# Kernel optimization log

Hardware: AMD Instinct MI355X
Metric: run time of the kernel (lower is better)

The kernel has to match this reference:

```python
import jax, jax.numpy as jnp
from jax import lax
import numpy as np

IGNORE_INDEX = -100


def setup_inputs() -> dict:
    key = jax.random.key(0)
    k1, k2, k3 = jax.random.split(key, 3)
    N, D, V = 8192, 2048, 32000
    x = jax.random.normal(k1, (N, D), dtype=jnp.float32) * (D ** -0.5)
    proj_weight = jax.random.normal(k2, (V, D), dtype=jnp.float32) * (D ** -0.5)
    target = jax.random.randint(k3, (N,), 0, V, dtype=jnp.int64 if jax.config.jax_enable_x64 else jnp.int32)
    return {"x": x, "proj_weight": proj_weight, "target": target, "num_splits": 4}


def reference(x, proj_weight, target, num_splits):
    # Fused linear-projection + cross-entropy, chunked over the token dim so the
    # full [N, V] logits tensor is never materialized (only [N/num_splits, V]).
    N, D = x.shape
    chunk = N // num_splits  # N chosen divisible by num_splits
    x_c = x.reshape(num_splits, chunk, D)
    t_c = target.reshape(num_splits, chunk)

    def body(carry, inp):
        loss_sum, count = carry
        xi, ti = inp  # [chunk, D], [chunk]
        logits = jnp.einsum('nd,vd->nv', xi, proj_weight)  # [chunk, V]
        lse = jax.nn.logsumexp(logits, axis=-1)            # [chunk]
        valid = ti != IGNORE_INDEX
        safe_t = jnp.where(valid, ti, 0)
        tgt_logit = jnp.take_along_axis(logits, safe_t[:, None], axis=-1)[:, 0]
        loss = jnp.where(valid, lse - tgt_logit, 0.0)
        return (loss_sum + loss.sum(), count + valid.sum()), None

    init = (jnp.float32(0.0), jnp.int32(0))
    (loss_sum, count), _ = lax.scan(body, init, (x_c, t_c))
    return loss_sum / count.astype(jnp.float32)  # mean over non-ignored tokens
```

## Files before the change

### kernel.cpp

```cpp
#include <hip/hip_runtime.h>
#include <hip/hip_bf16.h>


typedef __bf16 bf16_t;
typedef bf16_t bf16x8 __attribute__((ext_vector_type(8)));
typedef float f32x4 __attribute__((ext_vector_type(4)));

constexpr int N_TOK = 8192;
constexpr int DIM   = 2048;
constexpr int VOCAB = 32000;
constexpr int BM = 256, BN = 256, BK = 64;
constexpr int MT  = N_TOK / BM;
constexpr int NVT = VOCAB / BN;
constexpr int NKT = DIM / BK;
constexpr int IGNORE_INDEX = -100;

#define GPTR(p) ((const __attribute__((address_space(1))) void*)(p))
#define LPTR(p) ((__attribute__((address_space(3))) void*)(p))

#define VMCNT(N)                                            \
  asm volatile("s_waitcnt vmcnt(" #N ")" ::: "memory");     \
  __builtin_amdgcn_sched_barrier(0)
#define LGKM0()                                             \
  asm volatile("s_waitcnt lgkmcnt(0)" ::: "memory");        \
  __builtin_amdgcn_sched_barrier(0)

__device__ __forceinline__ bf16_t f2bf(float f) {
  union { float f; unsigned u; } in; in.f = f;
  unsigned u = in.u;
  unsigned r = u + 0x7fffu + ((u >> 16) & 1u);
  union { unsigned short s; bf16_t b; } out;
  out.s = (unsigned short)(r >> 16);
  return out.b;
}

constexpr int XN8 = N_TOK * DIM / 8;
constexpr int WN8 = VOCAB * DIM / 8;
constexpr int CVT_BLOCKS = 2048;

__global__ __launch_bounds__(256) void cvt_both(const float* __restrict__ x,
                                                const float* __restrict__ w,
                                                bf16_t* __restrict__ xb,
                                                bf16_t* __restrict__ wb) {
  for (int i = blockIdx.x * 256 + threadIdx.x; i < XN8 + WN8; i += CVT_BLOCKS * 256) {
    const float* src; bf16_t* dst; int j;
    if (i < XN8) { src = x; dst = xb; j = i; }
    else { src = w; dst = wb; j = i - XN8; }
    const float4* s = (const float4*)src;
    float4 a = s[2 * (size_t)j], b = s[2 * (size_t)j + 1];
    bf16x8 o;
    o[0] = f2bf(a.x); o[1] = f2bf(a.y); o[2] = f2bf(a.z); o[3] = f2bf(a.w);
    o[4] = f2bf(b.x); o[5] = f2bf(b.y); o[6] = f2bf(b.z); o[7] = f2bf(b.w);
    *(bf16x8*)(dst + (size_t)j * 8) = o;
  }
}

__device__ __forceinline__ void stage_half(const bf16_t* base, int kt,
                                           long toff, char* smem, int ldsoff,
                                           int tid) {
  const bf16_t* g = base + kt * BK + toff;
  __builtin_amdgcn_global_load_lds(GPTR(g), LPTR(smem + ldsoff + tid * 16), 16, 0, 0);
  __builtin_amdgcn_global_load_lds(GPTR(g + 64 * DIM), LPTR(smem + ldsoff + 8192 + tid * 16), 16, 0, 0);
}

template <int SLOT>
__device__ __forceinline__ bf16x8 ldA(const char* smem, int row, int ks, int lg) {
  int ch = (ks * 4 + lg) ^ (row & 7);
  return *(const bf16x8*)(smem + SLOT + row * 128 + ch * 16);
}
template <int SLOT>
__device__ __forceinline__ bf16x8 ldB(const char* smem, int row, int ks, int lg) {
  int ch = (ks * 4 + lg) ^ (row & 7);
  return *(const bf16x8*)(smem + SLOT + 32768 + row * 128 + ch * 16);
}

#define PRE_MFMA()                                    \
  __builtin_amdgcn_s_barrier();                       \
  LGKM0();

#define MFMA_HALF(MOFF)                                                         \
  __builtin_amdgcn_s_setprio(1);                                                \
  _Pragma("unroll") for (int m = 0; m < 4; ++m)                                 \
    _Pragma("unroll") for (int n = 0; n < 4; ++n)                               \
      acc[m + MOFF][n] = __builtin_amdgcn_mfma_f32_16x16x32_bf16(               \
          aq[m], bq[n], acc[m + MOFF][n], 0, 0, 0);                             \
  __builtin_amdgcn_s_setprio(0);

template <int CUR, int NXT>
__device__ __forceinline__ void tile_body(
    const bf16_t* Ab, const bf16_t* Bb, int ktB, int ktA2, long toff,
    char* smem, int tid, int wr, int wc, int l15, int lg, f32x4 (&acc)[8][4]) {
  bf16x8 aq[4], bq[4];
  const int arow = wr * 128 + l15;
  const int brow = wc * 64 + l15;

#pragma unroll
  for (int m = 0; m < 4; ++m) aq[m] = ldA<CUR>(smem, arow + m * 16, 0, lg);
#pragma unroll
  for (int n = 0; n < 4; ++n) bq[n] = ldB<CUR>(smem, brow + n * 16, 0, lg);
  stage_half(Bb, ktB, toff, smem, NXT + 32768, tid);
  VMCNT(4);
  PRE_MFMA();
  MFMA_HALF(0);
  __builtin_amdgcn_s_barrier();

#pragma unroll
  for (int m = 0; m < 4; ++m) aq[m] = ldA<CUR>(smem, arow + 64 + m * 16, 0, lg);
  stage_half(Bb + 128 * DIM, ktB, toff, smem, NXT + 49152, tid);
  PRE_MFMA();
  MFMA_HALF(4);
  __builtin_amdgcn_s_barrier();

#pragma unroll
  for (int m = 0; m < 4; ++m) aq[m] = ldA<CUR>(smem, arow + m * 16, 1, lg);
#pragma unroll
  for (int n = 0; n < 4; ++n) bq[n] = ldB<CUR>(smem, brow + n * 16, 1, lg);
  stage_half(Ab + 128 * DIM, ktB, toff, smem, NXT + 16384, tid);
  PRE_MFMA();
  MFMA_HALF(0);
  __builtin_amdgcn_s_barrier();

#pragma unroll
  for (int m = 0; m < 4; ++m) aq[m] = ldA<CUR>(smem, arow + 64 + m * 16, 1, lg);
  stage_half(Ab, ktA2, toff, smem, CUR, tid);
  VMCNT(4);
  PRE_MFMA();
  MFMA_HALF(4);
  __builtin_amdgcn_s_barrier();
}

__global__ __launch_bounds__(512, 2) void fused_gemm_lse(
    const bf16_t* __restrict__ X, const bf16_t* __restrict__ W,
    const int* __restrict__ target,
    float2* __restrict__ partials, float* __restrict__ tgt_logit) {
  __shared__ __align__(16) char smem[131072];

  const int tid  = threadIdx.x;
  const int lane = tid & 63;
  const int wid  = tid >> 6;
  const int wr   = wid >> 2;
  const int wc   = wid & 3;
  const int l15  = lane & 15;
  const int lg   = lane >> 4;

  int bid  = blockIdx.x;
  int wgid = (bid & 7) * (MT * NVT / 8) + (bid >> 3);
  int mt = wgid & (MT - 1);
  int vt = wgid >> 5;
  const int brow = mt * BM;
  const int bcol = vt * BN;

  const bf16_t* Abase = X + (size_t)brow * DIM;
  const bf16_t* Bbase = W + (size_t)bcol * DIM;

  const int srow = tid >> 3;
  const int ssc  = (tid & 7) ^ (srow & 7);
  const long toff = (long)srow * DIM + ssc * 8;

  f32x4 acc[8][4];
#pragma unroll
  for (int m = 0; m < 8; ++m)
#pragma unroll
    for (int n = 0; n < 4; ++n)
      acc[m][n] = (f32x4){0.f, 0.f, 0.f, 0.f};

  stage_half(Abase,             0, toff, smem, 0,     tid);
  stage_half(Abase + 128 * DIM, 0, toff, smem, 16384, tid);
  stage_half(Bbase,             0, toff, smem, 32768, tid);
  stage_half(Bbase + 128 * DIM, 0, toff, smem, 49152, tid);
  stage_half(Abase,             1, toff, smem, 65536, tid);
  VMCNT(0);
  __builtin_amdgcn_s_barrier();

  for (int t = 0; t < NKT; t += 2) {
    tile_body<0, 65536>(Abase, Bbase, (t + 1) & (NKT - 1), (t + 2) & (NKT - 1),
                        toff, smem, tid, wr, wc, l15, lg, acc);
    tile_body<65536, 0>(Abase, Bbase, (t + 2) & (NKT - 1), (t + 3) & (NKT - 1),
                        toff, smem, tid, wr, wc, l15, lg, acc);
  }

  __syncthreads();
  float* smax = (float*)smem;
  float* ssum = (float*)(smem + 4096);
#pragma unroll
  for (int m = 0; m < 8; ++m) {
#pragma unroll
    for (int i = 0; i < 4; ++i) {
      int rloc = wr * 128 + m * 16 + lg * 4 + i;
      int grow = brow + rloc;
      int tgt  = target[grow];
      float v0 = acc[m][0][i], v1 = acc[m][1][i], v2 = acc[m][2][i], v3 = acc[m][3][i];
      int colbase = bcol + wc * 64 + l15;
      if (colbase      == tgt) tgt_logit[grow] = v0;
      if (colbase + 16 == tgt) tgt_logit[grow] = v1;
      if (colbase + 32 == tgt) tgt_logit[grow] = v2;
      if (colbase + 48 == tgt) tgt_logit[grow] = v3;
      float rmax = fmaxf(fmaxf(v0, v1), fmaxf(v2, v3));
#pragma unroll
      for (int s = 1; s < 16; s <<= 1) rmax = fmaxf(rmax, __shfl_xor(rmax, s));
      float rsum = __expf(v0 - rmax) + __expf(v1 - rmax) +
                   __expf(v2 - rmax) + __expf(v3 - rmax);
#pragma unroll
      for (int s = 1; s < 16; s <<= 1) rsum += __shfl_xor(rsum, s);
      if (l15 == 0) { smax[rloc * 4 + wc] = rmax; ssum[rloc * 4 + wc] = rsum; }
    }
  }
  __syncthreads();
  if (tid < BM) {
    float M = smax[tid * 4], S = ssum[tid * 4];
#pragma unroll
    for (int c = 1; c < 4; ++c) {
      float m2 = smax[tid * 4 + c], s2 = ssum[tid * 4 + c];
      float Mn = fmaxf(M, m2);
      S = S * __expf(M - Mn) + s2 * __expf(m2 - Mn);
      M = Mn;
    }
    partials[(size_t)(brow + tid) * NVT + vt] = make_float2(M, S);
  }
}

__global__ __launch_bounds__(256) void finalize_rows(
    const float2* __restrict__ partials, const float* __restrict__ tgt_logit,
    const int* __restrict__ target, float2* __restrict__ blocksum) {
  int tid = threadIdx.x, lane = tid & 63, w = tid >> 6;
  int row = blockIdx.x * 4 + w;
  float M = -1e30f, S = 0.f;
  for (int i = lane; i < NVT; i += 64) {
    float2 p = partials[(size_t)row * NVT + i];
    float Mn = fmaxf(M, p.x);
    S = S * __expf(M - Mn) + p.y * __expf(p.x - Mn);
    M = Mn;
  }
#pragma unroll
  for (int s = 1; s < 64; s <<= 1) {
    float Mo = __shfl_xor(M, s), So = __shfl_xor(S, s);
    float Mn = fmaxf(M, Mo);
    S = S * __expf(M - Mn) + So * __expf(Mo - Mn);
    M = Mn;
  }
  __shared__ float ls[4], cs[4];
  if (lane == 0) {
    int t = target[row];
    bool valid = (t != IGNORE_INDEX);
    float lse = M + __logf(S);
    ls[w] = valid ? (lse - tgt_logit[row]) : 0.f;
    cs[w] = valid ? 1.f : 0.f;
  }
  __syncthreads();
  if (tid == 0)
    blocksum[blockIdx.x] = make_float2(ls[0] + ls[1] + ls[2] + ls[3],
                                       cs[0] + cs[1] + cs[2] + cs[3]);
}

__global__ __launch_bounds__(256) void finalize_out(
    const float2* __restrict__ blocksum, float* __restrict__ out) {
  int tid = threadIdx.x;
  float s = 0.f, c = 0.f;
  for (int i = tid; i < N_TOK / 4; i += 256) {
    float2 b = blocksum[i];
    s += b.x; c += b.y;
  }
#pragma unroll
  for (int k = 1; k < 64; k <<= 1) { s += __shfl_xor(s, k); c += __shfl_xor(c, k); }
  __shared__ float ss[4], cc[4];
  int w = tid >> 6;
  if ((tid & 63) == 0) { ss[w] = s; cc[w] = c; }
  __syncthreads();
  if (tid == 0) out[0] = (ss[0] + ss[1] + ss[2] + ss[3]) / (cc[0] + cc[1] + cc[2] + cc[3]);
}

extern "C" void kernel_launch(void* const* d_in, const int* in_sizes, int n_in,
                              void* d_out, int out_size, void* d_ws, size_t ws_size,
                              hipStream_t stream) {
  const float* x = (const float*)d_in[0];
  const float* w = (const float*)d_in[1];
  const int* target = (const int*)d_in[2];
  float* out = (float*)d_out;

  char* ws = (char*)d_ws;
  size_t off = 0;
  bf16_t* Xbf = (bf16_t*)(ws + off); off += (size_t)N_TOK * DIM * 2;
  bf16_t* Wbf = (bf16_t*)(ws + off); off += (size_t)VOCAB * DIM * 2;
  float2* partials = (float2*)(ws + off); off += (size_t)N_TOK * NVT * 8;
  float*  tgtlog   = (float*)(ws + off);  off += (size_t)N_TOK * 4;
  float2* blocksum = (float2*)(ws + off); off += (size_t)(N_TOK / 4) * 8;
  (void)ws_size; (void)in_sizes; (void)n_in; (void)out_size;

  cvt_both<<<CVT_BLOCKS, 256, 0, stream>>>(x, w, Xbf, Wbf);
  fused_gemm_lse<<<MT * NVT, 512, 0, stream>>>(Xbf, Wbf, target, partials, tgtlog);
  finalize_rows<<<N_TOK / 4, 256, 0, stream>>>(partials, tgtlog, target, blocksum);
  finalize_out<<<1, 256, 0, stream>>>(blocksum, out);
}
```

Before: 1.441 ms.

## Replace interleaved 4-phase pipeline with simple double-buffered full-tile loads

Replaces the fine-grained four-phase schedule, which interleaved partial LDS reads, half-tile global-to-LDS stages and MFMA groups, with a simpler scheme. Each iteration reads the whole K tile from LDS into registers, issues all 64 MFMAs, then stages the entire next-but-one tile into the freed buffer. Barriers and waitcnt stalls drop from four per tile to one, but register pressure rises (24 bf16x8 fragments held at once) and the overlap between global loads and compute becomes coarser.

New measurement: 1.535 ms. 1.07x slower.

```diff
diff --git a/kernel.cpp b/kernel.cpp
--- a/kernel.cpp
+++ b/kernel.cpp
@@ -74,58 +74,38 @@
   return *(const bf16x8*)(smem + SLOT + 32768 + row * 128 + ch * 16);
 }
 
-#define PRE_MFMA()                                    \
-  __builtin_amdgcn_s_barrier();                       \
+template <int CUR>
+__device__ __forceinline__ void tile_body(
+    const bf16_t* Ab, const bf16_t* Bb, int ktN, long toff, char* smem,
+    int tid, int arow, int brow, int lg, f32x4 (&acc)[8][4]) {
+  bf16x8 a0[8], b0[4], a1[8], b1[4];
+#pragma unroll
+  for (int m = 0; m < 8; ++m) a0[m] = ldA<CUR>(smem, arow + m * 16, 0, lg);
+#pragma unroll
+  for (int n = 0; n < 4; ++n) b0[n] = ldB<CUR>(smem, brow + n * 16, 0, lg);
+#pragma unroll
+  for (int m = 0; m < 8; ++m) a1[m] = ldA<CUR>(smem, arow + m * 16, 1, lg);
+#pragma unroll
+  for (int n = 0; n < 4; ++n) b1[n] = ldB<CUR>(smem, brow + n * 16, 1, lg);
+  __builtin_amdgcn_s_setprio(1);
+#pragma unroll
+  for (int m = 0; m < 8; ++m)
+#pragma unroll
+    for (int n = 0; n < 4; ++n)
+      acc[m][n] = __builtin_amdgcn_mfma_f32_16x16x32_bf16(a0[m], b0[n], acc[m][n], 0, 0, 0);
+#pragma unroll
+  for (int m = 0; m < 8; ++m)
+#pragma unroll
+    for (int n = 0; n < 4; ++n)
+      acc[m][n] = __builtin_amdgcn_mfma_f32_16x16x32_bf16(a1[m], b1[n], acc[m][n], 0, 0, 0);
+  __builtin_amdgcn_s_setprio(0);
   LGKM0();
-
-#define MFMA_HALF(MOFF)                                                         \
-  __builtin_amdgcn_s_setprio(1);                                                \
-  _Pragma("unroll") for (int m = 0; m < 4; ++m)                                 \
-    _Pragma("unroll") for (int n = 0; n < 4; ++n)                               \
-      acc[m + MOFF][n] = __builtin_amdgcn_mfma_f32_16x16x32_bf16(               \
-          aq[m], bq[n], acc[m + MOFF][n], 0, 0, 0);                             \
-  __builtin_amdgcn_s_setprio(0);
-
-template <int CUR, int NXT>
-__device__ __forceinline__ void tile_body(
-    const bf16_t* Ab, const bf16_t* Bb, int ktB, int ktA2, long toff,
-    char* smem, int tid, int wr, int wc, int l15, int lg, f32x4 (&acc)[8][4]) {
-  bf16x8 aq[4], bq[4];
-  const int arow = wr * 128 + l15;
-  const int brow = wc * 64 + l15;
-
-#pragma unroll
-  for (int m = 0; m < 4; ++m) aq[m] = ldA<CUR>(smem, arow + m * 16, 0, lg);
-#pragma unroll
-  for (int n = 0; n < 4; ++n) bq[n] = ldB<CUR>(smem, brow + n * 16, 0, lg);
-  stage_half(Bb, ktB, toff, smem, NXT + 32768, tid);
-  VMCNT(4);
-  PRE_MFMA();
-  MFMA_HALF(0);
   __builtin_amdgcn_s_barrier();
-
-#pragma unroll
-  for (int m = 0; m < 4; ++m) aq[m] = ldA<CUR>(smem, arow + 64 + m * 16, 0, lg);
-  stage_half(Bb + 128 * DIM, ktB, toff, smem, NXT + 49152, tid);
-  PRE_MFMA();
-  MFMA_HALF(4);
-  __builtin_amdgcn_s_barrier();
-
-#pragma unroll
-  for (int m = 0; m < 4; ++m) aq[m] = ldA<CUR>(smem, arow + m * 16, 1, lg);
-#pragma unroll
-  for (int n = 0; n < 4; ++n) bq[n] = ldB<CUR>(smem, brow + n * 16, 1, lg);
-  stage_half(Ab + 128 * DIM, ktB, toff, smem, NXT + 16384, tid);
-  PRE_MFMA();
-  MFMA_HALF(0);
-  __builtin_amdgcn_s_barrier();
-
-#pragma unroll
-  for (int m = 0; m < 4; ++m) aq[m] = ldA<CUR>(smem, arow + 64 + m * 16, 1, lg);
-  stage_half(Ab, ktA2, toff, smem, CUR, tid);
-  VMCNT(4);
-  PRE_MFMA();
-  MFMA_HALF(4);
+  stage_half(Ab,             ktN, toff, smem, CUR,         tid);
+  stage_half(Ab + 128 * DIM, ktN, toff, smem, CUR + 16384, tid);
+  stage_half(Bb,             ktN, toff, smem, CUR + 32768, tid);
+  stage_half(Bb + 128 * DIM, ktN, toff, smem, CUR + 49152, tid);
+  VMCNT(8);
   __builtin_amdgcn_s_barrier();
 }
 
@@ -142,16 +122,18 @@
   const int wc   = wid & 3;
   const int l15  = lane & 15;
   const int lg   = lane >> 4;
+  const int arow = wr * 128 + l15;
+  const int brow = wc * 64 + l15;
 
   int bid  = blockIdx.x;
   int wgid = (bid & 7) * (MT * NVT / 8) + (bid >> 3);
   int mt = wgid & (MT - 1);
   int vt = wgid >> 5;
-  const int brow = mt * BM;
-  const int bcol = vt * BN;
-
-  const bf16_t* Abase = X + (size_t)brow * DIM;
-  const bf16_t* Bbase = W + (size_t)bcol * DIM;
+  const int brow_g = mt * BM;
+  const int bcol_g = vt * BN;
+
+  const bf16_t* Abase = X + (size_t)brow_g * DIM;
+  const bf16_t* Bbase = W + (size_t)bcol_g * DIM;
 
   const int srow = tid >> 3;
   const int ssc  = (tid & 7) ^ (srow & 7);
@@ -164,19 +146,20 @@
     for (int n = 0; n < 4; ++n)
       acc[m][n] = (f32x4){0.f, 0.f, 0.f, 0.f};
 
-  stage_half(Abase,             0, toff, smem, 0,     tid);
-  stage_half(Abase + 128 * DIM, 0, toff, smem, 16384, tid);
-  stage_half(Bbase,             0, toff, smem, 32768, tid);
-  stage_half(Bbase + 128 * DIM, 0, toff, smem, 49152, tid);
-  stage_half(Abase,             1, toff, smem, 65536, tid);
-  VMCNT(0);
+  stage_half(Abase,             0, toff, smem, 0,             tid);
+  stage_half(Abase + 128 * DIM, 0, toff, smem, 16384,         tid);
+  stage_half(Bbase,             0, toff, smem, 32768,         tid);
+  stage_half(Bbase + 128 * DIM, 0, toff, smem, 49152,         tid);
+  stage_half(Abase,             1, toff, smem, 65536,         tid);
+  stage_half(Abase + 128 * DIM, 1, toff, smem, 65536 + 16384, tid);
+  stage_half(Bbase,             1, toff, smem, 65536 + 32768, tid);
+  stage_half(Bbase + 128 * DIM, 1, toff, smem, 65536 + 49152, tid);
+  VMCNT(8);
   __builtin_amdgcn_s_barrier();
 
   for (int t = 0; t < NKT; t += 2) {
-    tile_body<0, 65536>(Abase, Bbase, (t + 1) & (NKT - 1), (t + 2) & (NKT - 1),
-                        toff, smem, tid, wr, wc, l15, lg, acc);
-    tile_body<65536, 0>(Abase, Bbase, (t + 2) & (NKT - 1), (t + 3) & (NKT - 1),
-                        toff, smem, tid, wr, wc, l15, lg, acc);
+    tile_body<0>(Abase, Bbase, (t + 2) & (NKT - 1), toff, smem, tid, arow, brow, lg, acc);
+    tile_body<65536>(Abase, Bbase, (t + 3) & (NKT - 1), toff, smem, tid, arow, brow, lg, acc);
   }
 
   __syncthreads();
@@ -187,10 +170,10 @@
 #pragma unroll
     for (int i = 0; i < 4; ++i) {
       int rloc = wr * 128 + m * 16 + lg * 4 + i;
-      int grow = brow + rloc;
+      int grow = brow_g + rloc;
       int tgt  = target[grow];
       float v0 = acc[m][0][i], v1 = acc[m][1][i], v2 = acc[m][2][i], v3 = acc[m][3][i];
-      int colbase = bcol + wc * 64 + l15;
+      int colbase = bcol_g + wc * 64 + l15;
       if (colbase      == tgt) tgt_logit[grow] = v0;
       if (colbase + 16 == tgt) tgt_logit[grow] = v1;
       if (colbase + 32 == tgt) tgt_logit[grow] = v2;
@@ -215,7 +198,7 @@
       S = S * __expf(M - Mn) + s2 * __expf(m2 - Mn);
       M = Mn;
     }
-    partials[(size_t)(brow + tid) * NVT + vt] = make_float2(M, S);
+    partials[(size_t)(brow_g + tid) * NVT + vt] = make_float2(M, S);
   }
 }
 
```
